# Kernel tuning notes

Measured on AMD Instinct MI355X. Metric: run time of the kernel, lower is better.

The kernel has to match this reference:

```python
import jax, jax.numpy as jnp
import numpy as np

N_HEAD = 8  # config.n_head

def _ln(x, g, b):
    # eqx.nn.LayerNorm, eps=1e-5
    m = x.mean(-1, keepdims=True)
    v = ((x - m) ** 2).mean(-1, keepdims=True)
    return (x - m) / jnp.sqrt(v + 1e-5) * g + b

def _lin(x, w, b):
    # eqx.nn.Linear: weight [out, in]
    return x @ w.T + b

def _heads(t):
    B, T, C = t.shape
    return t.reshape(B, T, N_HEAD, C // N_HEAD).transpose(0, 2, 1, 3)  # [B,H,T,d]

def _merge(t):
    B, H, T, d = t.shape
    return t.transpose(0, 2, 1, 3).reshape(B, T, H * d)

def setup_inputs() -> dict:
    key = jax.random.key(0)
    B, T1, T2, C, INNER, NIN = 4, 4096, 4096, 512, 2048, 2
    ks = jax.random.split(key, 16)
    w = lambda k, *s: 0.02 * jax.random.normal(k, s, dtype=jnp.float32)
    return {
        'x': jax.random.normal(ks[0], (B, T1, C), dtype=jnp.float32),
        'ys': jax.random.normal(ks[1], (NIN, B, T2, C), dtype=jnp.float32),
        'ln1_g': jnp.ones((C,)), 'ln1_b': jnp.zeros((C,)),
        'ln2_g': jnp.ones((NIN, C)), 'ln2_b': jnp.zeros((NIN, C)),
        'ln3_g': jnp.ones((C,)), 'ln3_b': jnp.zeros((C,)),
        'ln4_g': jnp.ones((C,)), 'ln4_b': jnp.zeros((C,)),
        'ln5_g': jnp.ones((C,)), 'ln5_b': jnp.zeros((C,)),
        'ca_wq': w(ks[2], C, C), 'ca_bq': jnp.zeros((C,)),
        'ca_wk': w(ks[3], NIN, C, C), 'ca_bk': jnp.zeros((NIN, C)),
        'ca_wv': w(ks[4], NIN, C, C), 'ca_bv': jnp.zeros((NIN, C)),
        'ca_wo': w(ks[5], C, C), 'ca_bo': jnp.zeros((C,)),
        'sa_wq': w(ks[6], C, C), 'sa_bq': jnp.zeros((C,)),
        'sa_wk': w(ks[7], C, C), 'sa_bk': jnp.zeros((C,)),
        'sa_wv': w(ks[8], C, C), 'sa_bv': jnp.zeros((C,)),
        'sa_wo': w(ks[9], C, C), 'sa_bo': jnp.zeros((C,)),
        'ffn1_w1': w(ks[10], INNER, C), 'ffn1_b1': jnp.zeros((INNER,)),
        'ffn1_w2': w(ks[11], C, INNER), 'ffn1_b2': jnp.zeros((C,)),
        'ffn2_w1': w(ks[12], INNER, C), 'ffn2_b1': jnp.zeros((INNER,)),
        'ffn2_w2': w(ks[13], C, INNER), 'ffn2_b2': jnp.zeros((C,)),
    }

def reference(x, ys, ln1_g, ln1_b, ln2_g, ln2_b, ln3_g, ln3_b, ln4_g, ln4_b, ln5_g, ln5_b,
              ca_wq, ca_bq, ca_wk, ca_bk, ca_wv, ca_bv, ca_wo, ca_bo,
              sa_wq, sa_bq, sa_wk, sa_bk, sa_wv, sa_bv, sa_wo, sa_bo,
              ffn1_w1, ffn1_b1, ffn1_w2, ffn1_b2, ffn2_w1, ffn2_b1, ffn2_w2, ffn2_b2):
    n_inputs = ys.shape[0]
    # ---- linear cross attention ----
    xn = _ln(x, ln1_g, ln1_b)
    q = jax.nn.softmax(_heads(_lin(xn, ca_wq, ca_bq)), axis=-1)  # [B,H,T1,d]
    out = q
    for i in range(n_inputs):  # small fixed branch count
        yn = _ln(ys[i], ln2_g[i], ln2_b[i])
        k = jax.nn.softmax(_heads(_lin(yn, ca_wk[i], ca_bk[i])), axis=-1)  # [B,H,T2,d]
        v = _heads(_lin(yn, ca_wv[i], ca_bv[i]))
        k_sum = k.sum(axis=-2, keepdims=True)                       # [B,H,1,d]
        D_inv = 1.0 / ((q * k_sum).sum(axis=-1, keepdims=True) + 1e-8)
        ctx = jnp.einsum('bhnd,bhnv->bhdv', k, v)                   # [B,H,d,d]
        out = out + jnp.einsum('bhqd,bhdv->bhqv', q, ctx) * D_inv
    x = x + _lin(_merge(out), ca_wo, ca_bo)
    # ---- FFN 1 ----
    xn = _ln(x, ln3_g, ln3_b)
    x = x + _lin(jax.nn.gelu(_lin(xn, ffn1_w1, ffn1_b1)), ffn1_w2, ffn1_b2)
    # ---- linear self attention (attn_type='l1') ----
    xn = _ln(x, ln4_g, ln4_b)
    q = jax.nn.softmax(_heads(_lin(xn, sa_wq, sa_bq)), axis=-1)
    k = jax.nn.softmax(_heads(_lin(xn, sa_wk, sa_bk)), axis=-1)
    v = _heads(_lin(xn, sa_wv, sa_bv))
    k_sum = k.sum(axis=-2, keepdims=True)
    D_inv = 1.0 / (q * k_sum).sum(axis=-1, keepdims=True)  # no eps in 'l1' branch
    ctx = jnp.einsum('bhnd,bhnv->bhdv', k, v)
    sa = jnp.einsum('bhqd,bhdv->bhqv', q, ctx) * D_inv + q
    x = x + _lin(_merge(sa), sa_wo, sa_bo)
    # ---- FFN 2 ----
    xn = _ln(x, ln5_g, ln5_b)
    x = x + _lin(jax.nn.gelu(_lin(xn, ffn2_w1, ffn2_b1)), ffn2_w2, ffn2_b2)
    return x
```

## Files before the change

kernel.cpp:

```cpp
#include <hip/hip_runtime.h>
#include <hip/hip_bf16.h>
#include <math.h>
#include <stdint.h>

typedef unsigned short u16;
typedef __attribute__((ext_vector_type(8))) short bh8;
typedef __attribute__((ext_vector_type(4))) float fx4;

#define DEV static __device__ __forceinline__

DEV float bf2f(u16 u){ union{unsigned u; float f;} v; v.u = ((unsigned)u)<<16; return v.f; }
DEV u16 f2bf(float f){ union{float f; unsigned u;} v; v.f = f;
  return (u16)((v.u + 0x7fffu + ((v.u>>16)&1u))>>16); }

DEV void async16(const u16* g, u16* l){
  __builtin_amdgcn_global_load_lds((__attribute__((address_space(1))) void*)(uintptr_t)g,
                                   (__attribute__((address_space(3))) void*)l, 16, 0, 0);
}

DEV float gelu_fast(float x){
  float x2 = x*x;
  float t  = __builtin_fmaf(x2, -0.071354816f, -1.5957691216f);
  float e  = __expf(x*t);
  return __fdividef(x, 1.f + e);
}

DEV int2 xcd_swz(){
  const int gx  = gridDim.x;
  const int ord = blockIdx.y*gx + blockIdx.x;
  const int nwg = gx*gridDim.y;
  const int wg  = (ord&7)*(nwg>>3) + (ord>>3);
  int2 r; r.x = wg % gx; r.y = wg / gx; return r;
}

struct WDesc { const float* src[14]; int off[14]; };
__global__ __launch_bounds__(256) void convw_kernel(WDesc d, u16* __restrict__ dst){
  int i = blockIdx.x*256 + threadIdx.x;
  int s = 0;
  #pragma unroll
  for(int j=1;j<14;j++) if(i >= d.off[j]) s = j;
  dst[i] = f2bf(d.src[s][i - d.off[s]]);
}

DEV float wsum64(float s){
  s += __shfl_xor(s,1,64);  s += __shfl_xor(s,2,64);  s += __shfl_xor(s,4,64);
  s += __shfl_xor(s,8,64);  s += __shfl_xor(s,16,64); s += __shfl_xor(s,32,64);
  return s;
}
DEV void ln_row(const float* xrow, const float* g, const float* bta, u16* orow, int lane){
  const float4* xr = (const float4*)xrow + lane*2;
  float4 a = xr[0], c = xr[1];
  float s = a.x+a.y+a.z+a.w + c.x+c.y+c.z+c.w;
  float mean = wsum64(s) * (1.f/512.f);
  float d0=a.x-mean,d1=a.y-mean,d2=a.z-mean,d3=a.w-mean;
  float d4=c.x-mean,d5=c.y-mean,d6=c.z-mean,d7=c.w-mean;
  float sv = d0*d0+d1*d1+d2*d2+d3*d3+d4*d4+d5*d5+d6*d6+d7*d7;
  float rstd = rsqrtf(wsum64(sv)*(1.f/512.f) + 1e-5f);
  const float4* gr = (const float4*)g   + lane*2;
  const float4* br = (const float4*)bta + lane*2;
  float4 g0=gr[0], g1=gr[1], b0=br[0], b1=br[1];
  bh8 o;
  o[0]=(short)f2bf(d0*rstd*g0.x+b0.x); o[1]=(short)f2bf(d1*rstd*g0.y+b0.y);
  o[2]=(short)f2bf(d2*rstd*g0.z+b0.z); o[3]=(short)f2bf(d3*rstd*g0.w+b0.w);
  o[4]=(short)f2bf(d4*rstd*g1.x+b1.x); o[5]=(short)f2bf(d5*rstd*g1.y+b1.y);
  o[6]=(short)f2bf(d6*rstd*g1.z+b1.z); o[7]=(short)f2bf(d7*rstd*g1.w+b1.w);
  *(bh8*)(orow + lane*8) = o;
}
__global__ __launch_bounds__(256) void ln_kernel(const float* __restrict__ x,
    const float* __restrict__ g, const float* __restrict__ bta, u16* __restrict__ out){
  int row  = blockIdx.x*4 + (threadIdx.x>>6);
  ln_row(x + (size_t)row*512, g, bta, out + (size_t)row*512, threadIdx.x&63);
}
__global__ __launch_bounds__(256) void lny_kernel(const float* __restrict__ ys,
    const float* __restrict__ g2, const float* __restrict__ b2, u16* __restrict__ out){
  int row  = blockIdx.x*4 + (threadIdx.x>>6);
  int i = row>>14;
  ln_row(ys + (size_t)row*512, g2 + i*512, b2 + i*512, out + (size_t)row*512, threadIdx.x&63);
}

#define GEMM_STAGE(Ab, Wb, K, kk, buf)                                               \
    async16(Ab + (size_t)srow*(K)      + (kk) + scol, &lsA[buf][(w*32   )*32]);      \
    async16(Ab + (size_t)(srow+16)*(K) + (kk) + scol, &lsA[buf][(w*32+16)*32]);      \
    async16(Wb + (size_t)srow*(K)      + (kk) + scol, &lsB[buf][(w*32   )*32]);      \
    async16(Wb + (size_t)(srow+16)*(K) + (kk) + scol, &lsB[buf][(w*32+16)*32]);

#define GEMM_FRAG_MFMA(cur)                                                          \
    bh8 af[4], bfx[4];                                                               \
    _Pragma("unroll")                                                                \
    for(int t=0;t<4;t++){                                                            \
      af[t]  = *(const bh8*)&lsA[cur][(wm*64+t*16+l15)*32 + rsw*8];                  \
      bfx[t] = *(const bh8*)&lsB[cur][(wn*64+t*16+l15)*32 + rsw*8];                  \
    }                                                                                \
    _Pragma("unroll")                                                                \
    for(int mt=0;mt<4;mt++)                                                          \
      _Pragma("unroll")                                                              \
      for(int nt=0;nt<4;nt++)                                                        \
        acc[mt][nt] = __builtin_amdgcn_mfma_f32_16x16x32_bf16(af[mt], bfx[nt], acc[mt][nt], 0,0,0);

#define GEMM_KLOOP_CNT(Ab, Wb, K) {                                                  \
  const int srow = w*32 + (lane>>2);                                                 \
  const int scol = (((lane&3) ^ ((srow>>1)&3)) * 8);                                 \
  const int rsw  = ((l15>>1)&3) ^ quad;                                              \
  GEMM_STAGE(Ab, Wb, K, 0, 0)                                                        \
  const int NS = (K)>>5;                                                             \
  for(int j=0;j<NS;j++){                                                             \
    const int cur = j&1;                                                             \
    if(j+1<NS){                                                                      \
      GEMM_STAGE(Ab, Wb, K, (j+1)*32, cur^1)                                         \
      asm volatile("s_waitcnt vmcnt(4)" ::: "memory");                               \
    } else {                                                                         \
      asm volatile("s_waitcnt vmcnt(0)" ::: "memory");                               \
    }                                                                                \
    __builtin_amdgcn_s_barrier();                                                    \
    GEMM_FRAG_MFMA(cur)                                                              \
    __builtin_amdgcn_s_barrier();                                                    \
  } }

#define GEMM_KLOOP_SYNC(Ab, Wb, K) {                                                 \
  const int srow = w*32 + (lane>>2);                                                 \
  const int scol = (((lane&3) ^ ((srow>>1)&3)) * 8);                                 \
  const int rsw  = ((l15>>1)&3) ^ quad;                                              \
  GEMM_STAGE(Ab, Wb, K, 0, 0)                                                        \
  __syncthreads();                                                                   \
  for(int k0=0;k0<K;k0+=32){                                                         \
    const int cur = (k0>>5)&1;                                                       \
    if(k0+32 < K){ GEMM_STAGE(Ab, Wb, K, k0+32, cur^1) }                             \
    GEMM_FRAG_MFMA(cur)                                                              \
    __syncthreads();                                                                 \
  } }

#define GEMM_STAGE64(Ab, Wb, K, kk, buf)                                             \
    async16(Ab + (size_t)srow*(K)      + (kk) + scol,  &lsA[buf][(w*32   )*32]);     \
    async16(Ab + (size_t)(srow+16)*(K) + (kk) + scol,  &lsA[buf][(w*32+16)*32]);     \
    async16(Wb + (size_t)browB*(K)     + (kk) + scolB, &lsB[buf][(w*16)*32]);

#define GEMM_KLOOP_CNT64(Ab, Wb, K) {                                                \
  const int srow  = w*32 + (lane>>2);                                                \
  const int scol  = (((lane&3) ^ ((srow>>1)&3)) * 8);                                \
  const int browB = w*16 + (lane>>2);                                                \
  const int scolB = (((lane&3) ^ ((browB>>1)&3)) * 8);                               \
  const int rsw   = ((l15>>1)&3) ^ quad;                                             \
  GEMM_STAGE64(Ab, Wb, K, 0, 0)                                                      \
  const int NS = (K)>>5;                                                             \
  for(int j=0;j<NS;j++){                                                             \
    const int cur = j&1;                                                             \
    if(j+1<NS){                                                                      \
      GEMM_STAGE64(Ab, Wb, K, (j+1)*32, cur^1)                                       \
      asm volatile("s_waitcnt vmcnt(3)" ::: "memory");                               \
    } else {                                                                         \
      asm volatile("s_waitcnt vmcnt(0)" ::: "memory");                               \
    }                                                                                \
    __builtin_amdgcn_s_barrier();                                                    \
    bh8 af[2], bfx[4];                                                               \
    _Pragma("unroll")                                                                \
    for(int t=0;t<2;t++)                                                             \
      af[t]  = *(const bh8*)&lsA[cur][(w*32+t*16+l15)*32 + rsw*8];                   \
    _Pragma("unroll")                                                                \
    for(int t=0;t<4;t++)                                                             \
      bfx[t] = *(const bh8*)&lsB[cur][(t*16+l15)*32 + rsw*8];                        \
    _Pragma("unroll")                                                                \
    for(int mt=0;mt<2;mt++)                                                          \
      _Pragma("unroll")                                                              \
      for(int nt=0;nt<4;nt++)                                                        \
        acc[mt][nt] = __builtin_amdgcn_mfma_f32_16x16x32_bf16(af[mt], bfx[nt], acc[mt][nt], 0,0,0); \
    __builtin_amdgcn_s_barrier();                                                    \
  } }

struct SubD { const float* bias; u16* out; float* ksum; int mode; };
struct Subs3 { SubD s[3]; };
__global__ __launch_bounds__(256) void gemm_qkv(const u16* __restrict__ A,
    const u16* __restrict__ W, Subs3 subs, int K, int wstride, int bstride, int ksstride){
  __shared__ __align__(16) u16 lsA[2][128*32];
  __shared__ __align__(16) u16 lsB[2][128*32];
  const int tid = threadIdx.x, lane = tid&63, w = tid>>6;
  const int quad = lane>>4, l15 = lane&15;
  const int2 swz = xcd_swz();
  const int bn = swz.x, bm = swz.y;
  const int iset = bm>>7;
  const int wm = w&1, wn = w>>1;
  fx4 acc[4][4];
  #pragma unroll
  for(int i=0;i<4;i++)
    #pragma unroll
    for(int j=0;j<4;j++) acc[i][j] = (fx4){0.f,0.f,0.f,0.f};
  const u16* Ab = A + (size_t)bm*128*K;
  const u16* Wb = W + (size_t)iset*wstride + (size_t)bn*128*K;
  GEMM_KLOOP_CNT(Ab, Wb, K)
  const SubD sub = subs.s[bn>>2];
  const int colw = (bn&3)*128 + wn*64;
  const float* bias = sub.bias + iset*bstride;
  float bcol[4];
  #pragma unroll
  for(int nt=0;nt<4;nt++) bcol[nt] = bias[colw + nt*16 + l15];

  if(sub.mode==1){
    float ksacc[4] = {0.f,0.f,0.f,0.f};
    #pragma unroll
    for(int mt=0;mt<4;mt++)
      #pragma unroll
      for(int r=0;r<4;r++){
        float v0=acc[mt][0][r]+bcol[0], v1=acc[mt][1][r]+bcol[1];
        float v2=acc[mt][2][r]+bcol[2], v3=acc[mt][3][r]+bcol[3];
        float mx = fmaxf(fmaxf(v0,v1),fmaxf(v2,v3));
        mx = fmaxf(mx,__shfl_xor(mx,1,64)); mx = fmaxf(mx,__shfl_xor(mx,2,64));
        mx = fmaxf(mx,__shfl_xor(mx,4,64)); mx = fmaxf(mx,__shfl_xor(mx,8,64));
        float e0=__expf(v0-mx), e1=__expf(v1-mx), e2=__expf(v2-mx), e3=__expf(v3-mx);
        float s = e0+e1+e2+e3;
        s += __shfl_xor(s,1,64); s += __shfl_xor(s,2,64);
        s += __shfl_xor(s,4,64); s += __shfl_xor(s,8,64);
        float inv = __fdividef(1.f, s);
        e0*=inv; e1*=inv; e2*=inv; e3*=inv;
        ksacc[0]+=e0; ksacc[1]+=e1; ksacc[2]+=e2; ksacc[3]+=e3;
        int row = bm*128 + wm*64 + mt*16 + quad*4 + r;
        size_t rb = (size_t)row*512;
        sub.out[rb+colw+ 0+l15]=f2bf(e0); sub.out[rb+colw+16+l15]=f2bf(e1);
        sub.out[rb+colw+32+l15]=f2bf(e2); sub.out[rb+colw+48+l15]=f2bf(e3);
      }
    if(sub.ksum){
      int b = (bm&127)>>5;
      float* ks = sub.ksum + iset*ksstride + b*512;
      #pragma unroll
      for(int nt=0;nt<4;nt++){
        float s = ksacc[nt];
        s += __shfl_xor(s,16,64); s += __shfl_xor(s,32,64);
        if(quad==0) atomicAdd(&ks[colw + nt*16 + l15], s);
      }
    }
  } else {
    #pragma unroll
    for(int mt=0;mt<4;mt++)
      #pragma unroll
      for(int r=0;r<4;r++){
        int row = bm*128 + wm*64 + mt*16 + quad*4 + r;
        size_t rb = (size_t)row*512;
        #pragma unroll
        for(int nt=0;nt<4;nt++)
          sub.out[rb + colw + nt*16 + l15] = f2bf(acc[mt][nt][r] + bcol[nt]);
      }
  }
}

__global__ __launch_bounds__(256) void gemm_q64(const u16* __restrict__ A,
    const u16* __restrict__ W, const float* __restrict__ bias, u16* __restrict__ out){
  __shared__ __align__(16) u16 lsA[2][128*32];
  __shared__ __align__(16) u16 lsB[2][64*32];
  const int tid = threadIdx.x, lane = tid&63, w = tid>>6;
  const int quad = lane>>4, l15 = lane&15;
  const int2 swz = xcd_swz();
  const int bn = swz.x, bm = swz.y;
  fx4 acc[2][4];
  #pragma unroll
  for(int i=0;i<2;i++)
    #pragma unroll
    for(int j=0;j<4;j++) acc[i][j] = (fx4){0.f,0.f,0.f,0.f};
  const u16* Ab = A + (size_t)bm*128*512;
  const u16* Wb = W + (size_t)bn*64*512;
  GEMM_KLOOP_CNT64(Ab, Wb, 512)
  const int colb = bn*64;
  float bcol[4];
  #pragma unroll
  for(int nt=0;nt<4;nt++) bcol[nt] = bias[colb + nt*16 + l15];
  #pragma unroll
  for(int mt=0;mt<2;mt++)
    #pragma unroll
    for(int r=0;r<4;r++){
      float v0=acc[mt][0][r]+bcol[0], v1=acc[mt][1][r]+bcol[1];
      float v2=acc[mt][2][r]+bcol[2], v3=acc[mt][3][r]+bcol[3];
      float mx = fmaxf(fmaxf(v0,v1),fmaxf(v2,v3));
      mx = fmaxf(mx,__shfl_xor(mx,1,64)); mx = fmaxf(mx,__shfl_xor(mx,2,64));
      mx = fmaxf(mx,__shfl_xor(mx,4,64)); mx = fmaxf(mx,__shfl_xor(mx,8,64));
      float e0=__expf(v0-mx), e1=__expf(v1-mx), e2=__expf(v2-mx), e3=__expf(v3-mx);
      float s = e0+e1+e2+e3;
      s += __shfl_xor(s,1,64); s += __shfl_xor(s,2,64);
      s += __shfl_xor(s,4,64); s += __shfl_xor(s,8,64);
      float inv = __fdividef(1.f, s);
      e0*=inv; e1*=inv; e2*=inv; e3*=inv;
      int row = bm*128 + w*32 + mt*16 + quad*4 + r;
      size_t rb = (size_t)row*512;
      out[rb+colb+ 0+l15]=f2bf(e0); out[rb+colb+16+l15]=f2bf(e1);
      out[rb+colb+32+l15]=f2bf(e2); out[rb+colb+48+l15]=f2bf(e3);
    }
}

__global__ __launch_bounds__(256) void gemm_dn64(const u16* __restrict__ A,
    const u16* __restrict__ W, const float* __restrict__ bias,
    const float* __restrict__ res, float* __restrict__ out, int N, int K){
  __shared__ __align__(16) u16 lsA[2][128*32];
  __shared__ __align__(16) u16 lsB[2][64*32];
  const int tid = threadIdx.x, lane = tid&63, w = tid>>6;
  const int quad = lane>>4, l15 = lane&15;
  const int2 swz = xcd_swz();
  const int bn = swz.x, bm = swz.y;
  fx4 acc[2][4];
  #pragma unroll
  for(int i=0;i<2;i++)
    #pragma unroll
    for(int j=0;j<4;j++) acc[i][j] = (fx4){0.f,0.f,0.f,0.f};
  const u16* Ab = A + (size_t)bm*128*K;
  const u16* Wb = W + (size_t)bn*64*K;
  GEMM_KLOOP_CNT64(Ab, Wb, K)
  const int colb = bn*64;
  float bcol[4];
  #pragma unroll
  for(int nt=0;nt<4;nt++) bcol[nt] = bias[colb + nt*16 + l15];
  #pragma unroll
  for(int mt=0;mt<2;mt++)
    #pragma unroll
    for(int r=0;r<4;r++){
      int row = bm*128 + w*32 + mt*16 + quad*4 + r;
      size_t rb = (size_t)row*N;
      #pragma unroll
      for(int nt=0;nt<4;nt++){
        int col = colb + nt*16 + l15;
        out[rb+col] = res[rb+col] + acc[mt][nt][r] + bcol[nt];
      }
    }
}

__global__ __launch_bounds__(256) void gemm_up(const u16* __restrict__ A,
    const u16* __restrict__ W, const float* __restrict__ bias,
    u16* __restrict__ out, int N, int K){
  __shared__ __align__(16) u16 lsA[2][128*32];
  __shared__ __align__(16) u16 lsB[2][128*32];
  const int tid = threadIdx.x, lane = tid&63, w = tid>>6;
  const int quad = lane>>4, l15 = lane&15;
  const int2 swz = xcd_swz();
  const int bn = swz.x, bm = swz.y;
  const int wm = w&1, wn = w>>1;
  fx4 acc[4][4];
  #pragma unroll
  for(int i=0;i<4;i++)
    #pragma unroll
    for(int j=0;j<4;j++) acc[i][j] = (fx4){0.f,0.f,0.f,0.f};
  const u16* Ab = A + (size_t)bm*128*K;
  const u16* Wb = W + (size_t)bn*128*K;
  GEMM_KLOOP_SYNC(Ab, Wb, K)
  const int colbase = bn*128 + wn*64;
  float bcol[4];
  #pragma unroll
  for(int nt=0;nt<4;nt++) bcol[nt] = bias[colbase + nt*16 + l15];
  #pragma unroll
  for(int mt=0;mt<4;mt++)
    #pragma unroll
    for(int r=0;r<4;r++){
      int row = bm*128 + wm*64 + mt*16 + quad*4 + r;
      size_t rb = (size_t)row*N;
      #pragma unroll
      for(int nt=0;nt<4;nt++)
        out[rb + colbase + nt*16 + l15] = f2bf(gelu_fast(acc[mt][nt][r] + bcol[nt]));
    }
}

__global__ __launch_bounds__(256) void ctx_kernel(const u16* __restrict__ kb,
    const u16* __restrict__ vb, float* __restrict__ ctx, size_t kstride){
  __shared__ __align__(16) u16 lk[64*72];
  __shared__ __align__(16) u16 lv[64*72];
  const int tid=threadIdx.x, lane=tid&63, w=tid>>6, quad=lane>>4, l15=lane&15;
  const int bh2 = blockIdx.x, i = bh2>>5, h = bh2&7, b = (bh2>>3)&3;
  const u16* kbase = kb + (size_t)i*kstride;
  const u16* vbase = vb + (size_t)i*kstride;
  const size_t rowbase = (size_t)b*4096 + (size_t)blockIdx.y*512;
  const int mt0=(w&1)*32, nt0=(w>>1)*32;
  fx4 acc[2][2];
  #pragma unroll
  for(int x=0;x<2;x++)
    #pragma unroll
    for(int j=0;j<2;j++) acc[x][j] = (fx4){0.f,0.f,0.f,0.f};
  const int tl = tid>>2, part = tid&3;
  for(int it=0; it<8; it++){
    __syncthreads();
    {
      size_t gro = (rowbase + it*64 + tl)*512 + h*64 + part*16;
      bh8 k0 = *(const bh8*)(kbase + gro); bh8 k1 = *(const bh8*)(kbase + gro + 8);
      bh8 v0 = *(const bh8*)(vbase + gro); bh8 v1 = *(const bh8*)(vbase + gro + 8);
      #pragma unroll
      for(int j=0;j<8;j++){
        lk[(part*16+j  )*72 + tl] = (u16)k0[j];
        lk[(part*16+8+j)*72 + tl] = (u16)k1[j];
        lv[(part*16+j  )*72 + tl] = (u16)v0[j];
        lv[(part*16+8+j)*72 + tl] = (u16)v1[j];
      }
    }
// ... 71 lines not shown
    float dv[NIN][4];
    #pragma unroll
    for(int s=0;s<NIN;s++){
      float part = 0.f;
      #pragma unroll
      for(int j=0;j<8;j++)
        part += bf2f((u16)a0[j])*kslo[s][j] + bf2f((u16)a1[j])*kshi[s][j];
      part += __shfl_xor(part,16,64); part += __shfl_xor(part,32,64);
      #pragma unroll
      for(int r=0;r<4;r++)
        dv[s][r] = __fdividef(1.f, __shfl(part, quad*4+r, 64) + eps);
    }
    fx4 outv[4];
    #pragma unroll
    for(int nt=0;nt<4;nt++) outv[nt] = (fx4){0.f,0.f,0.f,0.f};
    #pragma unroll
    for(int s=0;s<=NIN;s++){
      fx4 c[4];
      #pragma unroll
      for(int nt=0;nt<4;nt++){
        c[nt] = (fx4){0.f,0.f,0.f,0.f};
        c[nt] = __builtin_amdgcn_mfma_f32_16x16x32_bf16(a0, bfr[s][nt][0], c[nt], 0,0,0);
        c[nt] = __builtin_amdgcn_mfma_f32_16x16x32_bf16(a1, bfr[s][nt][1], c[nt], 0,0,0);
      }
      #pragma unroll
      for(int nt=0;nt<4;nt++)
        #pragma unroll
        for(int r=0;r<4;r++) outv[nt][r] += c[nt][r]*((s==NIN)?1.f:dv[s][r]);
    }
    #pragma unroll
    for(int nt=0;nt<4;nt++)
      #pragma unroll
      for(int r=0;r<4;r++)
        out[(tb+quad*4+r)*512 + h*64 + nt*16 + l15] = f2bf(outv[nt][r]);
  }
}

extern "C" void kernel_launch(void* const* d_in, const int* in_sizes, int n_in,
                              void* d_out, int out_size, void* d_ws, size_t ws_size,
                              hipStream_t stream){
  const float* x_in =(const float*)d_in[0];
  const float* ys   =(const float*)d_in[1];
  const float* ln1g =(const float*)d_in[2],  *ln1b=(const float*)d_in[3];
  const float* ln2g =(const float*)d_in[4],  *ln2b=(const float*)d_in[5];
  const float* ln3g =(const float*)d_in[6],  *ln3b=(const float*)d_in[7];
  const float* ln4g =(const float*)d_in[8],  *ln4b=(const float*)d_in[9];
  const float* ln5g =(const float*)d_in[10], *ln5b=(const float*)d_in[11];
  const float* ca_wq=(const float*)d_in[12], *ca_bq=(const float*)d_in[13];
  const float* ca_wk=(const float*)d_in[14], *ca_bk=(const float*)d_in[15];
  const float* ca_wv=(const float*)d_in[16], *ca_bv=(const float*)d_in[17];
  const float* ca_wo=(const float*)d_in[18], *ca_bo=(const float*)d_in[19];
  const float* sa_wq=(const float*)d_in[20], *sa_bq=(const float*)d_in[21];
  const float* sa_wk=(const float*)d_in[22], *sa_bk=(const float*)d_in[23];
  const float* sa_wv=(const float*)d_in[24], *sa_bv=(const float*)d_in[25];
  const float* sa_wo=(const float*)d_in[26], *sa_bo=(const float*)d_in[27];
  const float* f1w1 =(const float*)d_in[28], *f1b1=(const float*)d_in[29];
  const float* f1w2 =(const float*)d_in[30], *f1b2=(const float*)d_in[31];
  const float* f2w1 =(const float*)d_in[32], *f2b1=(const float*)d_in[33];
  const float* f2w2 =(const float*)d_in[34], *f2b2=(const float*)d_in[35];

  char* p = (char*)d_ws;
  u16*   WBF = (u16*)p;    p += 13631488;
  float* XW  = (float*)p;  p += 33554432;
  u16*   XN2 = (u16*)p;    p += 33554432;
  u16*   QB  = (u16*)p;    p += 16777216;
  u16*   R1  = (u16*)p;    p += 67108864;
  u16*   OUTB= (u16*)p;    p += 16777216;
  float* SM  = (float*)p;  p += 1597440;
  u16*   XN  = XN2;
  u16*   KB2 = R1;
  u16*   VB2 = R1 + 16777216;
  u16*   HB  = R1;
  float* CTXC = SM;
  float* CTXS = SM + 262144;
  float* KSC  = SM + 393216;
  float* KSS  = SM + 397312;

  WDesc wd;
  const float* wsrc[14] = {ca_wq, ca_wk, ca_wv, ca_wk+262144, ca_wv+262144, ca_wo,
                           sa_wq, sa_wk, sa_wv, sa_wo, f1w1, f1w2, f2w1, f2w2};
  const int    woff[14] = {0, 262144, 524288, 786432, 1048576, 1310720,
                           1572864, 1835008, 2097152, 2359296,
                           2621440, 3670016, 4718592, 5767168};
  for(int i=0;i<14;i++){ wd.src[i]=wsrc[i]; wd.off[i]=woff[i]; }
  convw_kernel<<<26624,256,0,stream>>>(wd, WBF);
  hipMemsetAsync(SM, 0, 399360*sizeof(float), stream);

  SubD zsub = {nullptr,nullptr,nullptr,0};

  ln_kernel<<<4096,256,0,stream>>>(x_in, ln1g, ln1b, OUTB);
  lny_kernel<<<8192,256,0,stream>>>(ys, ln2g, ln2b, XN2);
  gemm_q64<<<dim3(8,128),256,0,stream>>>(OUTB, WBF+0, ca_bq, QB);
  { Subs3 s = {{ {ca_bk, KB2, KSC, 1}, {ca_bv, VB2, nullptr, 0}, zsub }};
    gemm_qkv<<<dim3(8,256),256,0,stream>>>(XN2, WBF+262144, s, 512,
                                           524288, 512, 2048); }
  ctx_kernel<<<dim3(64,8),256,0,stream>>>(KB2, VB2, CTXC, (size_t)16384*512);
  apply_kernel<2><<<dim3(32,16),256,0,stream>>>(QB, CTXC, KSC, 1e-8f, OUTB);
  gemm_dn64<<<dim3(8,128),256,0,stream>>>(OUTB, WBF+1310720, ca_bo, x_in, XW, 512, 512);

  ln_kernel<<<4096,256,0,stream>>>(XW, ln3g, ln3b, XN);
  gemm_up<<<dim3(16,128),256,0,stream>>>(XN, WBF+2621440, f1b1, HB, 2048, 512);
  gemm_dn64<<<dim3(8,128),256,0,stream>>>(HB, WBF+3670016, f1b2, XW, XW, 512, 2048);

  ln_kernel<<<4096,256,0,stream>>>(XW, ln4g, ln4b, XN);
  { Subs3 s = {{ {sa_bq, QB, nullptr, 1}, {sa_bk, KB2, KSS, 1}, {sa_bv, VB2, nullptr, 0} }};
    gemm_qkv<<<dim3(12,128),256,0,stream>>>(XN, WBF+1572864, s, 512, 0,0,0); }
  ctx_kernel<<<dim3(32,8),256,0,stream>>>(KB2, VB2, CTXS, 0);
  apply_kernel<1><<<dim3(32,16),256,0,stream>>>(QB, CTXS, KSS, 0.f, OUTB);
  gemm_dn64<<<dim3(8,128),256,0,stream>>>(OUTB, WBF+2359296, sa_bo, XW, XW, 512, 512);

  ln_kernel<<<4096,256,0,stream>>>(XW, ln5g, ln5b, XN);
  gemm_up<<<dim3(16,128),256,0,stream>>>(XN, WBF+4718592, f2b1, HB, 2048, 512);
  gemm_dn64<<<dim3(8,128),256,0,stream>>>(HB, WBF+5767168, f2b2, XW, (float*)d_out, 512, 2048);
}
```

Baseline: 709.7 us.

## Store activations in MFMA fragment layout and load A operands directly to registers

Producers (layernorm, gelu up-projection, attention output) now write bf16 activations in a 16-row blocked fragment layout instead of plain row-major. The GEMMs then load each wave's A fragments straight from global memory into registers, prefetched one K-step ahead, and no longer stage A through LDS. This removes the A-side LDS traffic and halves shared memory per block, which could raise occupancy. In exchange it adds extra outstanding global loads with retuned waitcnts, and every consumer of these buffers must agree on the new layout.

```diff
diff --git a/kernel.cpp b/kernel.cpp
--- a/kernel.cpp
+++ b/kernel.cpp
@@ -16,6 +16,11 @@
 DEV void async16(const u16* g, u16* l){
   __builtin_amdgcn_global_load_lds((__attribute__((address_space(1))) void*)(uintptr_t)g,
                                    (__attribute__((address_space(3))) void*)l, 16, 0, 0);
+}
+
+DEV size_t faddr(int row, int col, int Kbuf){
+  return (size_t)(row>>4)*((size_t)Kbuf*16)
+       + (size_t)((col>>3)*128 + (row&15)*8 + (col&7));
 }
 
 DEV float gelu_fast(float x){
@@ -64,113 +69,144 @@
   o[2]=(short)f2bf(d2*rstd*g0.z+b0.z); o[3]=(short)f2bf(d3*rstd*g0.w+b0.w);
   o[4]=(short)f2bf(d4*rstd*g1.x+b1.x); o[5]=(short)f2bf(d5*rstd*g1.y+b1.y);
   o[6]=(short)f2bf(d6*rstd*g1.z+b1.z); o[7]=(short)f2bf(d7*rstd*g1.w+b1.w);
-  *(bh8*)(orow + lane*8) = o;
+  *(bh8*)(orow + (size_t)lane*128) = o;
 }
 __global__ __launch_bounds__(256) void ln_kernel(const float* __restrict__ x,
     const float* __restrict__ g, const float* __restrict__ bta, u16* __restrict__ out){
   int row  = blockIdx.x*4 + (threadIdx.x>>6);
-  ln_row(x + (size_t)row*512, g, bta, out + (size_t)row*512, threadIdx.x&63);
+  u16* orow = out + (size_t)(row>>4)*8192 + (size_t)(row&15)*8;
+  ln_row(x + (size_t)row*512, g, bta, orow, threadIdx.x&63);
 }
 __global__ __launch_bounds__(256) void lny_kernel(const float* __restrict__ ys,
     const float* __restrict__ g2, const float* __restrict__ b2, u16* __restrict__ out){
   int row  = blockIdx.x*4 + (threadIdx.x>>6);
   int i = row>>14;
-  ln_row(ys + (size_t)row*512, g2 + i*512, b2 + i*512, out + (size_t)row*512, threadIdx.x&63);
-}
-
-#define GEMM_STAGE(Ab, Wb, K, kk, buf)                                               \
-    async16(Ab + (size_t)srow*(K)      + (kk) + scol, &lsA[buf][(w*32   )*32]);      \
-    async16(Ab + (size_t)(srow+16)*(K) + (kk) + scol, &lsA[buf][(w*32+16)*32]);      \
+  u16* orow = out + (size_t)(row>>4)*8192 + (size_t)(row&15)*8;
+  ln_row(ys + (size_t)row*512, g2 + i*512, b2 + i*512, orow, threadIdx.x&63);
+}
+
+#define BSTAGE128(Wb, K, kk, buf)                                                    \
     async16(Wb + (size_t)srow*(K)      + (kk) + scol, &lsB[buf][(w*32   )*32]);      \
     async16(Wb + (size_t)(srow+16)*(K) + (kk) + scol, &lsB[buf][(w*32+16)*32]);
 
-#define GEMM_FRAG_MFMA(cur)                                                          \
-    bh8 af[4], bfx[4];                                                               \
+#define APREF4(AF, K, kk)                                                            \
     _Pragma("unroll")                                                                \
-    for(int t=0;t<4;t++){                                                            \
-      af[t]  = *(const bh8*)&lsA[cur][(wm*64+t*16+l15)*32 + rsw*8];                  \
-      bfx[t] = *(const bh8*)&lsB[cur][(wn*64+t*16+l15)*32 + rsw*8];                  \
-    }                                                                                \
-    _Pragma("unroll")                                                                \
-    for(int mt=0;mt<4;mt++)                                                          \
+    for(int t=0;t<4;t++)                                                             \
+      AF[t] = *(const bh8*)(Alane + (size_t)t*16*(K) + (size_t)(kk)*16);
+
+#define MFMA128(AF, CUR)                                                             \
+    { bh8 bfx[4];                                                                    \
       _Pragma("unroll")                                                              \
-      for(int nt=0;nt<4;nt++)                                                        \
-        acc[mt][nt] = __builtin_amdgcn_mfma_f32_16x16x32_bf16(af[mt], bfx[nt], acc[mt][nt], 0,0,0);
-
-#define GEMM_KLOOP_CNT(Ab, Wb, K) {                                                  \
-  const int srow = w*32 + (lane>>2);                                                 \
-  const int scol = (((lane&3) ^ ((srow>>1)&3)) * 8);                                 \
-  const int rsw  = ((l15>>1)&3) ^ quad;                                              \
-  GEMM_STAGE(Ab, Wb, K, 0, 0)                                                        \
-  const int NS = (K)>>5;                                                             \
-  for(int j=0;j<NS;j++){                                                             \
-    const int cur = j&1;                                                             \
-    if(j+1<NS){                                                                      \
-      GEMM_STAGE(Ab, Wb, K, (j+1)*32, cur^1)                                         \
-      asm volatile("s_waitcnt vmcnt(4)" ::: "memory");                               \
+      for(int t=0;t<4;t++)                                                           \
+        bfx[t] = *(const bh8*)&lsB[CUR][(wn*64+t*16+l15)*32 + rsw*8];                \
+      _Pragma("unroll")                                                              \
+      for(int mt=0;mt<4;mt++)                                                        \
+        _Pragma("unroll")                                                            \
+        for(int nt=0;nt<4;nt++)                                                      \
+          acc[mt][nt] = __builtin_amdgcn_mfma_f32_16x16x32_bf16(AF[mt], bfx[nt], acc[mt][nt], 0,0,0); }
+
+#define CSTEP128(AFU, AFP, CUR, jj, Wb, K)                                           \
+    if((jj)+1<NS){                                                                   \
+      BSTAGE128(Wb, K, ((jj)+1)*32, (CUR)^1)                                         \
+      asm volatile("" ::: "memory");                                                 \
+      APREF4(AFP, K, ((jj)+1)*32)                                                    \
+      asm volatile("s_waitcnt vmcnt(10)" ::: "memory");                              \
     } else {                                                                         \
       asm volatile("s_waitcnt vmcnt(0)" ::: "memory");                               \
     }                                                                                \
     __builtin_amdgcn_s_barrier();                                                    \
-    GEMM_FRAG_MFMA(cur)                                                              \
-    __builtin_amdgcn_s_barrier();                                                    \
-  } }
-
-#define GEMM_KLOOP_SYNC(Ab, Wb, K) {                                                 \
+    MFMA128(AFU, CUR)                                                                \
+    __builtin_amdgcn_s_barrier();
+
+#define KLOOP_CNT128(Ab, Wb, K, WTILE)                                               \
   const int srow = w*32 + (lane>>2);                                                 \
   const int scol = (((lane&3) ^ ((srow>>1)&3)) * 8);                                 \
   const int rsw  = ((l15>>1)&3) ^ quad;                                              \
-  GEMM_STAGE(Ab, Wb, K, 0, 0)                                                        \
+  const u16* Alane = (Ab) + (size_t)(WTILE)*16*(K) + lane*8;                         \
+  bh8 afA[4], afB[4];                                                                \
+  BSTAGE128(Wb, K, 0, 0)                                                             \
+  asm volatile("" ::: "memory");                                                     \
+  APREF4(afA, K, 0)                                                                  \
+  const int NS = (K)>>5;                                                             \
+  for(int j=0;j<NS;j+=2){                                                            \
+    CSTEP128(afA, afB, 0, j,   Wb, K)                                                \
+    CSTEP128(afB, afA, 1, j+1, Wb, K)                                                \
+  }
+
+#define SSTEP128(AFU, AFP, CUR, jj, Wb, K)                                           \
+    if((jj)+1<NS){                                                                   \
+      BSTAGE128(Wb, K, ((jj)+1)*32, (CUR)^1)                                         \
+      APREF4(AFP, K, ((jj)+1)*32)                                                    \
+    }                                                                                \
+    MFMA128(AFU, CUR)                                                                \
+    __syncthreads();
+
+#define KLOOP_SYNC128(Ab, Wb, K, WTILE)                                              \
+  const int srow = w*32 + (lane>>2);                                                 \
+  const int scol = (((lane&3) ^ ((srow>>1)&3)) * 8);                                 \
+  const int rsw  = ((l15>>1)&3) ^ quad;                                              \
+  const u16* Alane = (Ab) + (size_t)(WTILE)*16*(K) + lane*8;                         \
+  bh8 afA[4], afB[4];                                                                \
+  BSTAGE128(Wb, K, 0, 0)                                                             \
+  APREF4(afA, K, 0)                                                                  \
   __syncthreads();                                                                   \
-  for(int k0=0;k0<K;k0+=32){                                                         \
-    const int cur = (k0>>5)&1;                                                       \
-    if(k0+32 < K){ GEMM_STAGE(Ab, Wb, K, k0+32, cur^1) }                             \
-    GEMM_FRAG_MFMA(cur)                                                              \
-    __syncthreads();                                                                 \
-  } }
-
-#define GEMM_STAGE64(Ab, Wb, K, kk, buf)                                             \
-    async16(Ab + (size_t)srow*(K)      + (kk) + scol,  &lsA[buf][(w*32   )*32]);     \
-    async16(Ab + (size_t)(srow+16)*(K) + (kk) + scol,  &lsA[buf][(w*32+16)*32]);     \
-    async16(Wb + (size_t)browB*(K)     + (kk) + scolB, &lsB[buf][(w*16)*32]);
-
-#define GEMM_KLOOP_CNT64(Ab, Wb, K) {                                                \
-  const int srow  = w*32 + (lane>>2);                                                \
-  const int scol  = (((lane&3) ^ ((srow>>1)&3)) * 8);                                \
-  const int browB = w*16 + (lane>>2);                                                \
-  const int scolB = (((lane&3) ^ ((browB>>1)&3)) * 8);                               \
-  const int rsw   = ((l15>>1)&3) ^ quad;                                             \
-  GEMM_STAGE64(Ab, Wb, K, 0, 0)                                                      \
   const int NS = (K)>>5;                                                             \
-  for(int j=0;j<NS;j++){                                                             \
-    const int cur = j&1;                                                             \
-    if(j+1<NS){                                                                      \
-      GEMM_STAGE64(Ab, Wb, K, (j+1)*32, cur^1)                                       \
-      asm volatile("s_waitcnt vmcnt(3)" ::: "memory");                               \
+  for(int j=0;j<NS;j+=2){                                                            \
+    SSTEP128(afA, afB, 0, j,   Wb, K)                                                \
+    SSTEP128(afB, afA, 1, j+1, Wb, K)                                                \
+  }
+
+#define BSTAGE64(Wb, K, kk, buf)                                                     \
+    async16(Wb + (size_t)browB*(K) + (kk) + scolB, &lsB[buf][(w*16)*32]);
+
+#define APREF2(AF, K, kk)                                                            \
+    _Pragma("unroll")                                                                \
+    for(int t=0;t<2;t++)                                                             \
+      AF[t] = *(const bh8*)(Alane + (size_t)t*16*(K) + (size_t)(kk)*16);
+
+#define MFMA64(AF, CUR)                                                              \
+    { bh8 bfx[4];                                                                    \
+      _Pragma("unroll")                                                              \
+      for(int t=0;t<4;t++)                                                           \
+        bfx[t] = *(const bh8*)&lsB[CUR][(t*16+l15)*32 + rsw*8];                      \
+      _Pragma("unroll")                                                              \
+      for(int mt=0;mt<2;mt++)                                                        \
+        _Pragma("unroll")                                                            \
+        for(int nt=0;nt<4;nt++)                                                      \
+          acc[mt][nt] = __builtin_amdgcn_mfma_f32_16x16x32_bf16(AF[mt], bfx[nt], acc[mt][nt], 0,0,0); }
+
+#define CSTEP64(AFU, AFP, CUR, jj, Wb, K)                                            \
+    if((jj)+1<NS){                                                                   \
+      BSTAGE64(Wb, K, ((jj)+1)*32, (CUR)^1)                                          \
+      asm volatile("" ::: "memory");                                                 \
+      APREF2(AFP, K, ((jj)+1)*32)                                                    \
+      asm volatile("s_waitcnt vmcnt(5)" ::: "memory");                               \
     } else {                                                                         \
       asm volatile("s_waitcnt vmcnt(0)" ::: "memory");                               \
     }                                                                                \
     __builtin_amdgcn_s_barrier();                                                    \
-    bh8 af[2], bfx[4];                                                               \
-    _Pragma("unroll")                                                                \
-    for(int t=0;t<2;t++)                                                             \
-      af[t]  = *(const bh8*)&lsA[cur][(w*32+t*16+l15)*32 + rsw*8];                   \
-    _Pragma("unroll")                                                                \
-    for(int t=0;t<4;t++)                                                             \
-      bfx[t] = *(const bh8*)&lsB[cur][(t*16+l15)*32 + rsw*8];                        \
-    _Pragma("unroll")                                                                \
-    for(int mt=0;mt<2;mt++)                                                          \
-      _Pragma("unroll")                                                              \
-      for(int nt=0;nt<4;nt++)                                                        \
-        acc[mt][nt] = __builtin_amdgcn_mfma_f32_16x16x32_bf16(af[mt], bfx[nt], acc[mt][nt], 0,0,0); \
-    __builtin_amdgcn_s_barrier();                                                    \
-  } }
+    MFMA64(AFU, CUR)                                                                 \
+    __builtin_amdgcn_s_barrier();
+
+#define KLOOP_CNT64(Ab, Wb, K)                                                       \
+  const int browB = w*16 + (lane>>2);                                                \
+  const int scolB = (((lane&3) ^ ((browB>>1)&3)) * 8);                               \
+  const int rsw   = ((l15>>1)&3) ^ quad;                                             \
+  const u16* Alane = (Ab) + (size_t)(w*2)*16*(K) + lane*8;                           \
+  bh8 afA[2], afB[2];                                                                \
+  BSTAGE64(Wb, K, 0, 0)                                                              \
+  asm volatile("" ::: "memory");                                                     \
+  APREF2(afA, K, 0)                                                                  \
+  const int NS = (K)>>5;                                                             \
+  for(int j=0;j<NS;j+=2){                                                            \
+    CSTEP64(afA, afB, 0, j,   Wb, K)                                                 \
+    CSTEP64(afB, afA, 1, j+1, Wb, K)                                                 \
+  }
 
 struct SubD { const float* bias; u16* out; float* ksum; int mode; };
 struct Subs3 { SubD s[3]; };
 __global__ __launch_bounds__(256) void gemm_qkv(const u16* __restrict__ A,
     const u16* __restrict__ W, Subs3 subs, int K, int wstride, int bstride, int ksstride){
-  __shared__ __align__(16) u16 lsA[2][128*32];
   __shared__ __align__(16) u16 lsB[2][128*32];
   const int tid = threadIdx.x, lane = tid&63, w = tid>>6;
   const int quad = lane>>4, l15 = lane&15;
@@ -185,7 +221,7 @@
     for(int j=0;j<4;j++) acc[i][j] = (fx4){0.f,0.f,0.f,0.f};
   const u16* Ab = A + (size_t)bm*128*K;
   const u16* Wb = W + (size_t)iset*wstride + (size_t)bn*128*K;
-  GEMM_KLOOP_CNT(Ab, Wb, K)
+  KLOOP_CNT128(Ab, Wb, K, wm*4)
   const SubD sub = subs.s[bn>>2];
   const int colw = (bn&3)*128 + wn*64;
   const float* bias = sub.bias + iset*bstride;
@@ -242,7 +278,6 @@
 
 __global__ __launch_bounds__(256) void gemm_q64(const u16* __restrict__ A,
     const u16* __restrict__ W, const float* __restrict__ bias, u16* __restrict__ out){
-  __shared__ __align__(16) u16 lsA[2][128*32];
   __shared__ __align__(16) u16 lsB[2][64*32];
   const int tid = threadIdx.x, lane = tid&63, w = tid>>6;
   const int quad = lane>>4, l15 = lane&15;
@@ -255,7 +290,7 @@
     for(int j=0;j<4;j++) acc[i][j] = (fx4){0.f,0.f,0.f,0.f};
   const u16* Ab = A + (size_t)bm*128*512;
   const u16* Wb = W + (size_t)bn*64*512;
-  GEMM_KLOOP_CNT64(Ab, Wb, 512)
+  KLOOP_CNT64(Ab, Wb, 512)
   const int colb = bn*64;
   float bcol[4];
   #pragma unroll
@@ -285,7 +320,6 @@
 __global__ __launch_bounds__(256) void gemm_dn64(const u16* __restrict__ A,
     const u16* __restrict__ W, const float* __restrict__ bias,
     const float* __restrict__ res, float* __restrict__ out, int N, int K){
-  __shared__ __align__(16) u16 lsA[2][128*32];
   __shared__ __align__(16) u16 lsB[2][64*32];
   const int tid = threadIdx.x, lane = tid&63, w = tid>>6;
   const int quad = lane>>4, l15 = lane&15;
@@ -298,7 +332,7 @@
     for(int j=0;j<4;j++) acc[i][j] = (fx4){0.f,0.f,0.f,0.f};
   const u16* Ab = A + (size_t)bm*128*K;
   const u16* Wb = W + (size_t)bn*64*K;
-  GEMM_KLOOP_CNT64(Ab, Wb, K)
+  KLOOP_CNT64(Ab, Wb, K)
   const int colb = bn*64;
   float bcol[4];
   #pragma unroll
@@ -320,7 +354,6 @@
 __global__ __launch_bounds__(256) void gemm_up(const u16* __restrict__ A,
     const u16* __restrict__ W, const float* __restrict__ bias,
     u16* __restrict__ out, int N, int K){
-  __shared__ __align__(16) u16 lsA[2][128*32];
   __shared__ __align__(16) u16 lsB[2][128*32];
   const int tid = threadIdx.x, lane = tid&63, w = tid>>6;
   const int quad = lane>>4, l15 = lane&15;
@@ -334,7 +367,7 @@
     for(int j=0;j<4;j++) acc[i][j] = (fx4){0.f,0.f,0.f,0.f};
   const u16* Ab = A + (size_t)bm*128*K;
   const u16* Wb = W + (size_t)bn*128*K;
-  GEMM_KLOOP_SYNC(Ab, Wb, K)
+  KLOOP_SYNC128(Ab, Wb, K, wm*4)
   const int colbase = bn*128 + wn*64;
   float bcol[4];
   #pragma unroll
@@ -344,10 +377,11 @@
     #pragma unroll
     for(int r=0;r<4;r++){
       int row = bm*128 + wm*64 + mt*16 + quad*4 + r;
-      size_t rb = (size_t)row*N;
-      #pragma unroll
-      for(int nt=0;nt<4;nt++)
-        out[rb + colbase + nt*16 + l15] = f2bf(gelu_fast(acc[mt][nt][r] + bcol[nt]));
+      #pragma unroll
+      for(int nt=0;nt<4;nt++){
+        int col = colbase + nt*16 + l15;
+        out[faddr(row, col, N)] = f2bf(gelu_fast(acc[mt][nt][r] + bcol[nt]));
+      }
     }
 }
 
@@ -485,7 +519,7 @@
     for(int nt=0;nt<4;nt++)
       #pragma unroll
       for(int r=0;r<4;r++)
-        out[(tb+quad*4+r)*512 + h*64 + nt*16 + l15] = f2bf(outv[nt][r]);
+        out[faddr((int)tb + quad*4 + r, h*64 + nt*16 + l15, 512)] = f2bf(outv[nt][r]);
   }
 }
 
```

After: 692.5 us. -2.4%, faster.

## Store GEMM operands in MFMA fragment-tiled layout and load directly to registers

Applied to the files above, without the earlier changes.

All bf16 GEMM operands (weights, LayerNorm outputs, attention outputs, FFN hidden) are now written in a 16-row × 8-column fragment-tiled layout, so each lane can load its MFMA fragment with one contiguous 16-byte global load. The GEMM k-loops drop LDS staging and barriers and instead double-buffer fragments in registers. This removes shared-memory traffic and synchronisation. The cost is that operands are no longer reused through LDS across waves, so global/L2 traffic per block rises, and register pressure grows.

```diff
diff --git a/kernel.cpp b/kernel.cpp
--- a/kernel.cpp
+++ b/kernel.cpp
@@ -13,9 +13,9 @@
 DEV u16 f2bf(float f){ union{float f; unsigned u;} v; v.f = f;
   return (u16)((v.u + 0x7fffu + ((v.u>>16)&1u))>>16); }
 
-DEV void async16(const u16* g, u16* l){
-  __builtin_amdgcn_global_load_lds((__attribute__((address_space(1))) void*)(uintptr_t)g,
-                                   (__attribute__((address_space(3))) void*)l, 16, 0, 0);
+DEV size_t faddr(int row, int col, int Kbuf){
+  return (size_t)(row>>4)*((size_t)Kbuf*16)
+       + (size_t)((col>>3)*128 + (row&15)*8 + (col&7));
 }
 
 DEV float gelu_fast(float x){
@@ -33,13 +33,16 @@
   int2 r; r.x = wg % gx; r.y = wg / gx; return r;
 }
 
-struct WDesc { const float* src[14]; int off[14]; };
+struct WDesc { const float* src[14]; int off[14]; int ksh[14]; };
 __global__ __launch_bounds__(256) void convw_kernel(WDesc d, u16* __restrict__ dst){
   int i = blockIdx.x*256 + threadIdx.x;
   int s = 0;
   #pragma unroll
   for(int j=1;j<14;j++) if(i >= d.off[j]) s = j;
-  dst[i] = f2bf(d.src[s][i - d.off[s]]);
+  int local = i - d.off[s];
+  int ksh = d.ksh[s];
+  int n = local >> ksh, k = local & ((1<<ksh)-1);
+  dst[d.off[s] + faddr(n, k, 1<<ksh)] = f2bf(d.src[s][local]);
 }
 
 DEV float wsum64(float s){
@@ -64,114 +67,74 @@
   o[2]=(short)f2bf(d2*rstd*g0.z+b0.z); o[3]=(short)f2bf(d3*rstd*g0.w+b0.w);
   o[4]=(short)f2bf(d4*rstd*g1.x+b1.x); o[5]=(short)f2bf(d5*rstd*g1.y+b1.y);
   o[6]=(short)f2bf(d6*rstd*g1.z+b1.z); o[7]=(short)f2bf(d7*rstd*g1.w+b1.w);
-  *(bh8*)(orow + lane*8) = o;
+  *(bh8*)(orow + (size_t)lane*128) = o;
 }
 __global__ __launch_bounds__(256) void ln_kernel(const float* __restrict__ x,
     const float* __restrict__ g, const float* __restrict__ bta, u16* __restrict__ out){
   int row  = blockIdx.x*4 + (threadIdx.x>>6);
-  ln_row(x + (size_t)row*512, g, bta, out + (size_t)row*512, threadIdx.x&63);
+  u16* orow = out + (size_t)(row>>4)*8192 + (size_t)(row&15)*8;
+  ln_row(x + (size_t)row*512, g, bta, orow, threadIdx.x&63);
 }
 __global__ __launch_bounds__(256) void lny_kernel(const float* __restrict__ ys,
     const float* __restrict__ g2, const float* __restrict__ b2, u16* __restrict__ out){
   int row  = blockIdx.x*4 + (threadIdx.x>>6);
   int i = row>>14;
-  ln_row(ys + (size_t)row*512, g2 + i*512, b2 + i*512, out + (size_t)row*512, threadIdx.x&63);
-}
-
-#define GEMM_STAGE(Ab, Wb, K, kk, buf)                                               \
-    async16(Ab + (size_t)srow*(K)      + (kk) + scol, &lsA[buf][(w*32   )*32]);      \
-    async16(Ab + (size_t)(srow+16)*(K) + (kk) + scol, &lsA[buf][(w*32+16)*32]);      \
-    async16(Wb + (size_t)srow*(K)      + (kk) + scol, &lsB[buf][(w*32   )*32]);      \
-    async16(Wb + (size_t)(srow+16)*(K) + (kk) + scol, &lsB[buf][(w*32+16)*32]);
-
-#define GEMM_FRAG_MFMA(cur)                                                          \
-    bh8 af[4], bfx[4];                                                               \
+  u16* orow = out + (size_t)(row>>4)*8192 + (size_t)(row&15)*8;
+  ln_row(ys + (size_t)row*512, g2 + i*512, b2 + i*512, orow, threadIdx.x&63);
+}
+
+#define PREF4(F, base, K, kk)                                                        \
     _Pragma("unroll")                                                                \
-    for(int t=0;t<4;t++){                                                            \
-      af[t]  = *(const bh8*)&lsA[cur][(wm*64+t*16+l15)*32 + rsw*8];                  \
-      bfx[t] = *(const bh8*)&lsB[cur][(wn*64+t*16+l15)*32 + rsw*8];                  \
-    }                                                                                \
+    for(int t=0;t<4;t++)                                                             \
+      F[t] = *(const bh8*)((base) + (size_t)t*16*(K) + (size_t)(kk)*16);
+#define PREF2(F, base, K, kk)                                                        \
+    _Pragma("unroll")                                                                \
+    for(int t=0;t<2;t++)                                                             \
+      F[t] = *(const bh8*)((base) + (size_t)t*16*(K) + (size_t)(kk)*16);
+
+#define MFMA_4x4(AF, BF)                                                             \
     _Pragma("unroll")                                                                \
     for(int mt=0;mt<4;mt++)                                                          \
       _Pragma("unroll")                                                              \
       for(int nt=0;nt<4;nt++)                                                        \
-        acc[mt][nt] = __builtin_amdgcn_mfma_f32_16x16x32_bf16(af[mt], bfx[nt], acc[mt][nt], 0,0,0);
-
-#define GEMM_KLOOP_CNT(Ab, Wb, K) {                                                  \
-  const int srow = w*32 + (lane>>2);                                                 \
-  const int scol = (((lane&3) ^ ((srow>>1)&3)) * 8);                                 \
-  const int rsw  = ((l15>>1)&3) ^ quad;                                              \
-  GEMM_STAGE(Ab, Wb, K, 0, 0)                                                        \
-  const int NS = (K)>>5;                                                             \
-  for(int j=0;j<NS;j++){                                                             \
-    const int cur = j&1;                                                             \
-    if(j+1<NS){                                                                      \
-      GEMM_STAGE(Ab, Wb, K, (j+1)*32, cur^1)                                         \
-      asm volatile("s_waitcnt vmcnt(4)" ::: "memory");                               \
-    } else {                                                                         \
-      asm volatile("s_waitcnt vmcnt(0)" ::: "memory");                               \
-    }                                                                                \
-    __builtin_amdgcn_s_barrier();                                                    \
-    GEMM_FRAG_MFMA(cur)                                                              \
-    __builtin_amdgcn_s_barrier();                                                    \
-  } }
-
-#define GEMM_KLOOP_SYNC(Ab, Wb, K) {                                                 \
-  const int srow = w*32 + (lane>>2);                                                 \
-  const int scol = (((lane&3) ^ ((srow>>1)&3)) * 8);                                 \
-  const int rsw  = ((l15>>1)&3) ^ quad;                                              \
-  GEMM_STAGE(Ab, Wb, K, 0, 0)                                                        \
-  __syncthreads();                                                                   \
-  for(int k0=0;k0<K;k0+=32){                                                         \
-    const int cur = (k0>>5)&1;                                                       \
-    if(k0+32 < K){ GEMM_STAGE(Ab, Wb, K, k0+32, cur^1) }                             \
-    GEMM_FRAG_MFMA(cur)                                                              \
-    __syncthreads();                                                                 \
-  } }
-
-#define GEMM_STAGE64(Ab, Wb, K, kk, buf)                                             \
-    async16(Ab + (size_t)srow*(K)      + (kk) + scol,  &lsA[buf][(w*32   )*32]);     \
-    async16(Ab + (size_t)(srow+16)*(K) + (kk) + scol,  &lsA[buf][(w*32+16)*32]);     \
-    async16(Wb + (size_t)browB*(K)     + (kk) + scolB, &lsB[buf][(w*16)*32]);
-
-#define GEMM_KLOOP_CNT64(Ab, Wb, K) {                                                \
-  const int srow  = w*32 + (lane>>2);                                                \
-  const int scol  = (((lane&3) ^ ((srow>>1)&3)) * 8);                                \
-  const int browB = w*16 + (lane>>2);                                                \
-  const int scolB = (((lane&3) ^ ((browB>>1)&3)) * 8);                               \
-  const int rsw   = ((l15>>1)&3) ^ quad;                                             \
-  GEMM_STAGE64(Ab, Wb, K, 0, 0)                                                      \
-  const int NS = (K)>>5;                                                             \
-  for(int j=0;j<NS;j++){                                                             \
-    const int cur = j&1;                                                             \
-    if(j+1<NS){                                                                      \
-      GEMM_STAGE64(Ab, Wb, K, (j+1)*32, cur^1)                                       \
-      asm volatile("s_waitcnt vmcnt(3)" ::: "memory");                               \
-    } else {                                                                         \
-      asm volatile("s_waitcnt vmcnt(0)" ::: "memory");                               \
-    }                                                                                \
-    __builtin_amdgcn_s_barrier();                                                    \
-    bh8 af[2], bfx[4];                                                               \
-    _Pragma("unroll")                                                                \
-    for(int t=0;t<2;t++)                                                             \
-      af[t]  = *(const bh8*)&lsA[cur][(w*32+t*16+l15)*32 + rsw*8];                   \
-    _Pragma("unroll")                                                                \
-    for(int t=0;t<4;t++)                                                             \
-      bfx[t] = *(const bh8*)&lsB[cur][(t*16+l15)*32 + rsw*8];                        \
+        acc[mt][nt] = __builtin_amdgcn_mfma_f32_16x16x32_bf16(AF[mt], BF[nt], acc[mt][nt], 0,0,0);
+#define MFMA_2x4(AF, BF)                                                             \
     _Pragma("unroll")                                                                \
     for(int mt=0;mt<2;mt++)                                                          \
       _Pragma("unroll")                                                              \
       for(int nt=0;nt<4;nt++)                                                        \
-        acc[mt][nt] = __builtin_amdgcn_mfma_f32_16x16x32_bf16(af[mt], bfx[nt], acc[mt][nt], 0,0,0); \
-    __builtin_amdgcn_s_barrier();                                                    \
-  } }
+        acc[mt][nt] = __builtin_amdgcn_mfma_f32_16x16x32_bf16(AF[mt], BF[nt], acc[mt][nt], 0,0,0);
+
+#define KLOOP128_RR(Ab, Wb, K)                                                       \
+  const u16* Alane = (Ab) + (size_t)(wm*4)*16*(K) + lane*8;                          \
+  const u16* Wlane = (Wb) + (size_t)(wn*4)*16*(K) + lane*8;                          \
+  bh8 aA[4], bA[4], aB[4], bB[4];                                                    \
+  PREF4(aA, Alane, K, 0) PREF4(bA, Wlane, K, 0)                                      \
+  const int NS = (K)>>5;                                                             \
+  for(int j=0;j<NS;j+=2){                                                            \
+    if(j+1<NS){ PREF4(aB, Alane, K, (j+1)*32) PREF4(bB, Wlane, K, (j+1)*32) }        \
+    MFMA_4x4(aA, bA)                                                                 \
+    if(j+2<NS){ PREF4(aA, Alane, K, (j+2)*32) PREF4(bA, Wlane, K, (j+2)*32) }        \
+    if(j+1<NS){ MFMA_4x4(aB, bB) }                                                   \
+  }
+
+#define KLOOP64_RR(Ab, Wb, K)                                                        \
+  const u16* Alane = (Ab) + (size_t)(w*2)*16*(K) + lane*8;                           \
+  const u16* Wlane = (Wb) + lane*8;                                                  \
+  bh8 aA[2], bA[4], aB[2], bB[4];                                                    \
+  PREF2(aA, Alane, K, 0) PREF4(bA, Wlane, K, 0)                                      \
+  const int NS = (K)>>5;                                                             \
+  for(int j=0;j<NS;j+=2){                                                            \
+    if(j+1<NS){ PREF2(aB, Alane, K, (j+1)*32) PREF4(bB, Wlane, K, (j+1)*32) }        \
+    MFMA_2x4(aA, bA)                                                                 \
+    if(j+2<NS){ PREF2(aA, Alane, K, (j+2)*32) PREF4(bA, Wlane, K, (j+2)*32) }        \
+    if(j+1<NS){ MFMA_2x4(aB, bB) }                                                   \
+  }
 
 struct SubD { const float* bias; u16* out; float* ksum; int mode; };
 struct Subs3 { SubD s[3]; };
 __global__ __launch_bounds__(256) void gemm_qkv(const u16* __restrict__ A,
     const u16* __restrict__ W, Subs3 subs, int K, int wstride, int bstride, int ksstride){
-  __shared__ __align__(16) u16 lsA[2][128*32];
-  __shared__ __align__(16) u16 lsB[2][128*32];
   const int tid = threadIdx.x, lane = tid&63, w = tid>>6;
   const int quad = lane>>4, l15 = lane&15;
   const int2 swz = xcd_swz();
@@ -185,7 +148,7 @@
     for(int j=0;j<4;j++) acc[i][j] = (fx4){0.f,0.f,0.f,0.f};
   const u16* Ab = A + (size_t)bm*128*K;
   const u16* Wb = W + (size_t)iset*wstride + (size_t)bn*128*K;
-  GEMM_KLOOP_CNT(Ab, Wb, K)
+  KLOOP128_RR(Ab, Wb, K)
   const SubD sub = subs.s[bn>>2];
   const int colw = (bn&3)*128 + wn*64;
   const float* bias = sub.bias + iset*bstride;
@@ -242,8 +205,6 @@
 
 __global__ __launch_bounds__(256) void gemm_q64(const u16* __restrict__ A,
     const u16* __restrict__ W, const float* __restrict__ bias, u16* __restrict__ out){
-  __shared__ __align__(16) u16 lsA[2][128*32];
-  __shared__ __align__(16) u16 lsB[2][64*32];
   const int tid = threadIdx.x, lane = tid&63, w = tid>>6;
   const int quad = lane>>4, l15 = lane&15;
   const int2 swz = xcd_swz();
@@ -255,7 +216,7 @@
     for(int j=0;j<4;j++) acc[i][j] = (fx4){0.f,0.f,0.f,0.f};
   const u16* Ab = A + (size_t)bm*128*512;
   const u16* Wb = W + (size_t)bn*64*512;
-  GEMM_KLOOP_CNT64(Ab, Wb, 512)
+  KLOOP64_RR(Ab, Wb, 512)
   const int colb = bn*64;
   float bcol[4];
   #pragma unroll
@@ -285,8 +246,6 @@
 __global__ __launch_bounds__(256) void gemm_dn64(const u16* __restrict__ A,
     const u16* __restrict__ W, const float* __restrict__ bias,
     const float* __restrict__ res, float* __restrict__ out, int N, int K){
-  __shared__ __align__(16) u16 lsA[2][128*32];
-  __shared__ __align__(16) u16 lsB[2][64*32];
   const int tid = threadIdx.x, lane = tid&63, w = tid>>6;
   const int quad = lane>>4, l15 = lane&15;
   const int2 swz = xcd_swz();
@@ -298,7 +257,7 @@
     for(int j=0;j<4;j++) acc[i][j] = (fx4){0.f,0.f,0.f,0.f};
   const u16* Ab = A + (size_t)bm*128*K;
   const u16* Wb = W + (size_t)bn*64*K;
-  GEMM_KLOOP_CNT64(Ab, Wb, K)
+  KLOOP64_RR(Ab, Wb, K)
   const int colb = bn*64;
   float bcol[4];
   #pragma unroll
@@ -320,8 +279,6 @@
 __global__ __launch_bounds__(256) void gemm_up(const u16* __restrict__ A,
     const u16* __restrict__ W, const float* __restrict__ bias,
     u16* __restrict__ out, int N, int K){
-  __shared__ __align__(16) u16 lsA[2][128*32];
-  __shared__ __align__(16) u16 lsB[2][128*32];
   const int tid = threadIdx.x, lane = tid&63, w = tid>>6;
   const int quad = lane>>4, l15 = lane&15;
   const int2 swz = xcd_swz();
@@ -334,7 +291,7 @@
     for(int j=0;j<4;j++) acc[i][j] = (fx4){0.f,0.f,0.f,0.f};
   const u16* Ab = A + (size_t)bm*128*K;
   const u16* Wb = W + (size_t)bn*128*K;
-  GEMM_KLOOP_SYNC(Ab, Wb, K)
+  KLOOP128_RR(Ab, Wb, K)
   const int colbase = bn*128 + wn*64;
   float bcol[4];
   #pragma unroll
@@ -344,10 +301,11 @@
     #pragma unroll
     for(int r=0;r<4;r++){
       int row = bm*128 + wm*64 + mt*16 + quad*4 + r;
-      size_t rb = (size_t)row*N;
-      #pragma unroll
-      for(int nt=0;nt<4;nt++)
-        out[rb + colbase + nt*16 + l15] = f2bf(gelu_fast(acc[mt][nt][r] + bcol[nt]));
+      #pragma unroll
+      for(int nt=0;nt<4;nt++){
+        int col = colbase + nt*16 + l15;
+        out[faddr(row, col, N)] = f2bf(gelu_fast(acc[mt][nt][r] + bcol[nt]));
+      }
     }
 }
 
@@ -485,7 +443,7 @@
     for(int nt=0;nt<4;nt++)
       #pragma unroll
       for(int r=0;r<4;r++)
-        out[(tb+quad*4+r)*512 + h*64 + nt*16 + l15] = f2bf(outv[nt][r]);
+        out[faddr((int)tb + quad*4 + r, h*64 + nt*16 + l15, 512)] = f2bf(outv[nt][r]);
   }
 }
 
@@ -535,7 +493,8 @@
   const int    woff[14] = {0, 262144, 524288, 786432, 1048576, 1310720,
                            1572864, 1835008, 2097152, 2359296,
                            2621440, 3670016, 4718592, 5767168};
-  for(int i=0;i<14;i++){ wd.src[i]=wsrc[i]; wd.off[i]=woff[i]; }
+  const int    wksh[14] = {9,9,9,9,9,9, 9,9,9,9, 9,11, 9,11};
+  for(int i=0;i<14;i++){ wd.src[i]=wsrc[i]; wd.off[i]=woff[i]; wd.ksh[i]=wksh[i]; }
   convw_kernel<<<26624,256,0,stream>>>(wd, WBF);
   hipMemsetAsync(SM, 0, 399360*sizeof(float), stream);
 
```

Measured after the change: 748.5 us. 5.5% more time.
